# Kernel optimization log

Hardware: AMD Instinct MI355X
Metric: run time of the kernel (lower is better)

The kernel has to match this reference:

```python
import jax, jax.numpy as jnp
import numpy as np

N = 500_000
D = 256
G = 1024


def setup_inputs() -> dict:
    key = jax.random.key(0)
    k1, k2, k3, k4, k5, k6 = jax.random.split(key, 6)
    x = jax.random.normal(k1, (N, D), dtype=jnp.float32)
    batch = jnp.sort(jax.random.randint(k2, (N,), 0, G).astype(jnp.int64))
    s = 1.0 / np.sqrt(D)
    W1 = jax.random.normal(k3, (D, D), dtype=jnp.float32) * s
    b1 = jax.random.normal(k4, (D,), dtype=jnp.float32) * 0.01
    W2 = jax.random.normal(k5, (D, 1), dtype=jnp.float32) * s
    b2 = jax.random.normal(k6, (1,), dtype=jnp.float32) * 0.01
    return {"x": x, "batch": batch, "num_graphs": G,
            "W1": W1, "b1": b1, "W2": W2, "b2": b2}


def reference(x, batch, num_graphs, W1, b1, W2, b2):
    # gate MLP: Linear -> Tanh -> Linear  => [N, 1]
    h = jnp.tanh(x @ W1 + b1)
    scores = (h @ W2 + b2)[:, 0]  # [N]
    # segment softmax over nodes grouped by graph id
    seg_max = jax.ops.segment_max(scores, batch, num_segments=num_graphs)  # [G]
    # empty segments give -inf max, but no node indexes them
    e = jnp.exp(scores - seg_max[batch])  # [N]
    denom = jax.ops.segment_sum(e, batch, num_segments=num_graphs)  # [G]
    attn = e / denom[batch]  # [N]
    weighted = x * attn[:, None]  # [N, D]
    # global_add_pool: scatter-add nodes into graphs
    return jax.ops.segment_sum(weighted, batch, num_segments=num_graphs)  # [G, D]
```

## Files before the change

kernel.cpp:

```cpp
#include <hip/hip_runtime.h>
#include <hip/hip_bf16.h>

#define D 256

typedef __attribute__((ext_vector_type(8))) short bf16x8;
typedef __attribute__((ext_vector_type(4))) float f32x4;

__device__ __forceinline__ unsigned short f2bf(float a) {
    unsigned int u = __float_as_uint(a);
    u = (u + 0x7fffu + ((u >> 16) & 1u)) >> 16;
    return (unsigned short)u;
}

__device__ __forceinline__ unsigned int cvt_pk_bf16(float a, float b) {
    unsigned int r;
    asm("v_cvt_pk_bf16_f32 %0, %1, %2" : "=v"(r) : "v"(a), "v"(b));
    return r;
}

__device__ __forceinline__ float fast_tanh(float v) {
    float a = __builtin_fabsf(v);
    float e = __builtin_amdgcn_exp2f(a * -2.88539008177793f);
    float t = (1.0f - e) * __builtin_amdgcn_rcpf(1.0f + e);
    return __builtin_copysignf(t, v);
}

__device__ __forceinline__ int xf_off(int c, int r, int q) {
    return ((c << 10) + (r << 5) + (q << 4)) ^ ((c & 3) << 5) ^ ((r & 4) << 2);
}

__global__ void pack_w1_k(const float* __restrict__ W1, unsigned short* __restrict__ W1p) {
    int p = blockIdx.x * 256 + threadIdx.x;
    int e  = p & 7;
    int l  = (p >> 3) & 63;
    int cb = (p >> 9) & 15;
    int kk = p >> 13;
    int k   = 32 * kk + 8 * (l >> 4) + e;
    int col = 16 * cb + (l & 15);
    W1p[p] = f2bf(W1[k * D + col]);
}

__global__ void zero_k(float* __restrict__ p, int n) {
    int i = blockIdx.x * 256 + threadIdx.x;
    if (i < n) p[i] = 0.f;
}

__global__ void __launch_bounds__(256, 4)
fused_k(const float* __restrict__ x,
        const unsigned short* __restrict__ W1p,
        const float* __restrict__ b1,
        const float* __restrict__ W2,
        const float* __restrict__ b2,
        const int* __restrict__ batch, int N,
        float* __restrict__ accb, float* __restrict__ den) {
    __shared__ __align__(16) float Xf[8192];
    __shared__ float red[4][256];
    __shared__ float scpart[4][32];
    __shared__ float erow[32];
    __shared__ int   bids[32];

    const int tid = threadIdx.x;
    const int w   = tid >> 6;
    const int l   = tid & 63;
    const int l15 = l & 15;
    const int g4  = l >> 4;
    const int row0 = blockIdx.x * 32;

    char* xb = reinterpret_cast<char*>(Xf);

    const float4* x4 = reinterpret_cast<const float4*>(x);
    const bool full = (row0 + 32 <= N);
    #pragma unroll
    for (int it = 0; it < 8; ++it) {
        int idx = it * 256 + tid;
        int r    = idx >> 6;
        int col4 = idx & 63;
        float4 v = make_float4(0.f, 0.f, 0.f, 0.f);
        if (full || row0 + r < N) v = x4[(size_t)(row0 + r) * 64 + col4];
        *reinterpret_cast<float4*>(xb + xf_off(col4 >> 1, r, col4 & 1)) = v;
    }
    if (tid < 32) bids[tid] = batch[min(row0 + tid, N - 1)];
    __syncthreads();

    f32x4 acc[2][4];
    #pragma unroll
    for (int m = 0; m < 2; ++m)
        #pragma unroll
        for (int n = 0; n < 4; ++n)
            acc[m][n] = (f32x4){0.f, 0.f, 0.f, 0.f};

    #pragma unroll
    for (int kk = 0; kk < 8; ++kk) {
        bf16x8 bfr[4];
        #pragma unroll
        for (int n = 0; n < 4; ++n) {
            const bf16x8* bp = reinterpret_cast<const bf16x8*>(
                W1p + (size_t)(((kk * 16) + (w * 4 + n)) * 64 + l) * 8);
            bfr[n] = *bp;
        }
        bf16x8 afr[2];
        #pragma unroll
        for (int m = 0; m < 2; ++m) {
            int r = 16 * m + l15;
            int c = 4 * kk + g4;
            int o0 = xf_off(c, r, 0);
            float4 f0 = *reinterpret_cast<const float4*>(xb + o0);
            float4 f1 = *reinterpret_cast<const float4*>(xb + (o0 ^ 16));
            uint4 u;
            u.x = cvt_pk_bf16(f0.x, f0.y);
            u.y = cvt_pk_bf16(f0.z, f0.w);
            u.z = cvt_pk_bf16(f1.x, f1.y);
            u.w = cvt_pk_bf16(f1.z, f1.w);
            afr[m] = *reinterpret_cast<bf16x8*>(&u);
        }
        #pragma unroll
        for (int m = 0; m < 2; ++m)
            #pragma unroll
            for (int n = 0; n < 4; ++n)
                acc[m][n] = __builtin_amdgcn_mfma_f32_16x16x32_bf16(afr[m], bfr[n], acc[m][n], 0, 0, 0);
    }

    float part[2][4];
    #pragma unroll
    for (int m = 0; m < 2; ++m)
        #pragma unroll
        for (int r = 0; r < 4; ++r) part[m][r] = 0.f;

    #pragma unroll
    for (int n = 0; n < 4; ++n) {
        int col = 64 * w + 16 * n + l15;
        float b1v = b1[col];
        float w2v = W2[col];
        #pragma unroll
        for (int m = 0; m < 2; ++m)
            #pragma unroll
            for (int r = 0; r < 4; ++r) {
                float h = fast_tanh(acc[m][n][r] + b1v);
                part[m][r] += h * w2v;
            }
    }

    #pragma unroll
    for (int m = 0; m < 2; ++m)
        #pragma unroll
        for (int r = 0; r < 4; ++r) {
            float p = part[m][r];
            p += __shfl_xor(p, 8, 16);
            p += __shfl_xor(p, 4, 16);
            p += __shfl_xor(p, 2, 16);
            p += __shfl_xor(p, 1, 16);
            if (l15 == 0) scpart[w][16 * m + 4 * g4 + r] = p;
        }
    __syncthreads();

    if (tid < 32) {
        float s = scpart[0][tid] + scpart[1][tid] + scpart[2][tid] + scpart[3][tid] + b2[0];
        erow[tid] = (row0 + tid < N)
                  ? __builtin_amdgcn_exp2f(s * 1.4426950408889634f)
                  : 0.f;
    }
    __syncthreads();

    const int g0 = bids[0], g1 = bids[31];
    const int pc = l >> 1;
    const int pq = l & 1;
    for (int g = g0; g <= g1; ++g) {
        float4 a = make_float4(0.f, 0.f, 0.f, 0.f);
        #pragma unroll
        for (int it = 0; it < 8; ++it) {
            int r = 4 * it + w;
            float e = (bids[r] == g) ? erow[r] : 0.f;
            float4 v = *reinterpret_cast<const float4*>(xb + xf_off(pc, r, pq));
            a.x += e * v.x;
            a.y += e * v.y;
            a.z += e * v.z;
            a.w += e * v.w;
        }
        red[w][l * 4 + 0] = a.x;
        red[w][l * 4 + 1] = a.y;
        red[w][l * 4 + 2] = a.z;
        red[w][l * 4 + 3] = a.w;
        __syncthreads();
        float s = red[0][tid] + red[1][tid] + red[2][tid] + red[3][tid];
        atomicAdd(&accb[(size_t)g * D + tid], s);
        if (w == 0) {
            float e = 0.f;
            if (l < 32) e = (bids[l] == g) ? erow[l] : 0.f;
            e += __shfl_xor(e, 32);
            e += __shfl_xor(e, 16);
            e += __shfl_xor(e, 8);
            e += __shfl_xor(e, 4);
            e += __shfl_xor(e, 2);
            e += __shfl_xor(e, 1);
            if (l == 0) atomicAdd(&den[g], e);
        }
        __syncthreads();
    }
}

__global__ void __launch_bounds__(256)
norm_k(const float* __restrict__ accb, const float* __restrict__ den,
       float* __restrict__ out) {
    int g = blockIdx.x;
    float dv = den[g];
    float inv = (dv > 0.f) ? 1.0f / dv : 0.f;
    out[(size_t)g * D + threadIdx.x] = accb[(size_t)g * D + threadIdx.x] * inv;
}

extern "C" void kernel_launch(void* const* d_in, const int* in_sizes, int n_in,
                              void* d_out, int out_size, void* d_ws, size_t ws_size,
                              hipStream_t stream) {
    const float* x     = (const float*)d_in[0];
    const int*   batch = (const int*)d_in[1];
    const float* W1    = (const float*)d_in[3];
    const float* b1    = (const float*)d_in[4];
    const float* W2    = (const float*)d_in[5];
    const float* b2    = (const float*)d_in[6];
    float* out = (float*)d_out;

    const int N = in_sizes[0] / D;
    const int G = out_size / D;

    char* ws = (char*)d_ws;
    unsigned short* W1p = (unsigned short*)ws;
    float* accb = (float*)(ws + 131072);
    float* den  = (float*)(ws + 131072 + (size_t)G * D * 4);

    zero_k<<<dim3((G * D + G + 255) / 256), dim3(256), 0, stream>>>(accb, G * D + G);
    pack_w1_k<<<dim3(256), dim3(256), 0, stream>>>(W1, W1p);
    fused_k<<<dim3((N + 31) / 32), dim3(256), 0, stream>>>(x, W1p, b1, W2, b2, batch, N, accb, den);
    norm_k<<<dim3(G), dim3(256), 0, stream>>>(accb, den, out);
}
```

Measured before the change: 226.7 us.

## Persistent fused kernel with double-buffered async x loads and cross-tile segment accumulation

Replaces the one-block-per-32-rows launch with a persistent grid of 512 blocks, each walking a contiguous range of tiles. W1 fragments, b1 and W2 are loaded into registers once per block, and the next tile of x is prefetched into a second LDS buffer through direct global-to-LDS loads while the current tile runs its MFMA work. Pooling partials carry across tiles and are flushed with atomics only when the graph id changes, which cuts the number of atomics and barriers per tile. The cost is higher register pressure from 32 resident B fragments and 64KB of LDS, which lowers occupancy to 2 blocks per CU, plus more complex barrier logic.

```diff
diff --git a/kernel.cpp b/kernel.cpp
--- a/kernel.cpp
+++ b/kernel.cpp
@@ -1,7 +1,8 @@
 #include <hip/hip_runtime.h>
-#include <hip/hip_bf16.h>
 
 #define D 256
+#define ROWS 32
+#define NBLK 512
 
 typedef __attribute__((ext_vector_type(8))) short bf16x8;
 typedef __attribute__((ext_vector_type(4))) float f32x4;
@@ -27,6 +28,12 @@
 
 __device__ __forceinline__ int xf_off(int c, int r, int q) {
     return ((c << 10) + (r << 5) + (q << 4)) ^ ((c & 3) << 5) ^ ((r & 4) << 2);
+}
+
+__device__ __forceinline__ void gload_lds16(const void* g, void* l) {
+    __builtin_amdgcn_global_load_lds(
+        (const __attribute__((address_space(1))) unsigned int*)g,
+        (__attribute__((address_space(3))) unsigned int*)l, 16, 0, 0);
 }
 
 __global__ void pack_w1_k(const float* __restrict__ W1, unsigned short* __restrict__ W1p) {
@@ -45,157 +52,222 @@
     if (i < n) p[i] = 0.f;
 }
 
-__global__ void __launch_bounds__(256, 4)
+#define STAGE(XN, tn) do {                                                      \
+    const int _r0s = (tn) * ROWS;                                               \
+    _Pragma("unroll")                                                           \
+    for (int _it = 0; _it < 8; ++_it) {                                         \
+        const int _c = _it * 4 + w;                                             \
+        const int _r = (l >> 1) ^ (_c & 3);                                     \
+        const int _q = (l & 1) ^ ((_r >> 2) & 1);                               \
+        int _row = _r0s + _r; _row = (_row < N) ? _row : (N - 1);               \
+        gload_lds16((const char*)x + ((size_t)_row << 10) + (size_t)(((_c << 1) + _q) << 4), \
+                    (char*)(XN) + (_it << 12) + (w << 10) + (l << 4));          \
+    }                                                                           \
+} while (0)
+
+#define FLUSHX() do {                                                           \
+    *reinterpret_cast<float4*>(&red[w][l * 4]) = a4;                            \
+    int _m8 = 0x7fffffff;                                                       \
+    _Pragma("unroll")                                                           \
+    for (int _it = 0; _it < 8; ++_it)                                           \
+        if (bg[_it] > g_cur && bg[_it] < _m8) _m8 = bg[_it];                    \
+    _m8 = min(_m8, __shfl_xor(_m8, 1));  _m8 = min(_m8, __shfl_xor(_m8, 2));    \
+    _m8 = min(_m8, __shfl_xor(_m8, 4));  _m8 = min(_m8, __shfl_xor(_m8, 8));    \
+    _m8 = min(_m8, __shfl_xor(_m8, 16)); _m8 = min(_m8, __shfl_xor(_m8, 32));   \
+    float _dw = den_p;                                                          \
+    _dw += __shfl_xor(_dw, 1);  _dw += __shfl_xor(_dw, 2);                      \
+    _dw += __shfl_xor(_dw, 4);  _dw += __shfl_xor(_dw, 8);                      \
+    _dw += __shfl_xor(_dw, 16); _dw += __shfl_xor(_dw, 32);                     \
+    if (l == 0) { gmin4[w] = _m8; denw[w] = _dw; }                              \
+    asm volatile("s_waitcnt lgkmcnt(0)" ::: "memory");                          \
+    __builtin_amdgcn_sched_barrier(0);                                          \
+    __builtin_amdgcn_s_barrier();                                               \
+    __builtin_amdgcn_sched_barrier(0);                                          \
+    { const float _fs = red[0][tid] + red[1][tid] + red[2][tid] + red[3][tid];  \
+      atomicAdd(&accb[(size_t)g_cur * D + tid], _fs); }                         \
+    if (tid == 0)                                                               \
+        atomicAdd(&den[g_cur], (denw[0] + denw[1] + denw[2] + denw[3]) * 0.015625f); \
+    gnv = min(min(gmin4[0], gmin4[1]), min(gmin4[2], gmin4[3]));                \
+    a4 = make_float4(0.f, 0.f, 0.f, 0.f); den_p = 0.f;                          \
+    __builtin_amdgcn_s_barrier();                                               \
+    __builtin_amdgcn_sched_barrier(0);                                          \
+} while (0)
+
+#define POOL(XC) do {                                                           \
+    if (g_cur < 0) g_cur = g0u;                                                 \
+    while (true) {                                                              \
+        _Pragma("unroll")                                                       \
+        for (int _it = 0; _it < 8; ++_it) {                                     \
+            const int _r = 4 * _it + w;                                         \
+            const float _e = (bg[_it] == g_cur) ? erow[_r] : 0.f;               \
+            const float4 _v = *reinterpret_cast<const float4*>(                 \
+                (const char*)(XC) + xf_off(l >> 1, _r, l & 1));                 \
+            a4.x += _e * _v.x; a4.y += _e * _v.y;                               \
+            a4.z += _e * _v.z; a4.w += _e * _v.w;                               \
+            den_p += _e;                                                        \
+        }                                                                       \
+        if (glast <= g_cur) break;                                              \
+        FLUSHX();                                                               \
+        g_cur = gnv;                                                            \
+    }                                                                           \
+} while (0)
+
+#define BODY(XC, XN) do {                                                       \
+    const int _row0 = t * ROWS;                                                 \
+    _Pragma("unroll")                                                           \
+    for (int _it = 0; _it < 8; ++_it) {                                         \
+        int _ri = _row0 + 4 * _it + w;                                          \
+        bg[_it] = batch[_ri < N ? _ri : N - 1];                                 \
+    }                                                                           \
+    const int g0u = batch[_row0];                                               \
+    int _gli = _row0 + 31;                                                      \
+    const int glast = batch[_gli < N ? _gli : N - 1];                           \
+    __builtin_amdgcn_sched_barrier(0);                                          \
+    const bool _hn = (t + 1 < t1);                                              \
+    if (_hn) {                                                                  \
+        STAGE(XN, t + 1);                                                       \
+        asm volatile("s_waitcnt vmcnt(8) lgkmcnt(0)" ::: "memory");             \
+    } else {                                                                    \
+        asm volatile("s_waitcnt vmcnt(0) lgkmcnt(0)" ::: "memory");             \
+    }                                                                           \
+    __builtin_amdgcn_sched_barrier(0);                                          \
+    __builtin_amdgcn_s_barrier();                                               \
+    __builtin_amdgcn_sched_barrier(0);                                          \
+     \
+    f32x4 acc[2][4];                                                            \
+    _Pragma("unroll")                                                           \
+    for (int _m = 0; _m < 2; ++_m)                                              \
+        _Pragma("unroll")                                                       \
+        for (int _n = 0; _n < 4; ++_n) acc[_m][_n] = (f32x4){0.f, 0.f, 0.f, 0.f}; \
+    _Pragma("unroll")                                                           \
+    for (int _kk = 0; _kk < 8; ++_kk) {                                         \
+        bf16x8 _afr[2];                                                         \
+        _Pragma("unroll")                                                       \
+        for (int _m = 0; _m < 2; ++_m) {                                        \
+            const int _rr = 16 * _m + l15;                                      \
+            const int _cc = 4 * _kk + g4;                                       \
+            const int _o0 = xf_off(_cc, _rr, 0);                                \
+            const float4 _f0 = *reinterpret_cast<const float4*>((const char*)(XC) + _o0); \
+            const float4 _f1 = *reinterpret_cast<const float4*>((const char*)(XC) + (_o0 ^ 16)); \
+            uint4 _u;                                                           \
+            _u.x = cvt_pk_bf16(_f0.x, _f0.y); _u.y = cvt_pk_bf16(_f0.z, _f0.w); \
+            _u.z = cvt_pk_bf16(_f1.x, _f1.y); _u.w = cvt_pk_bf16(_f1.z, _f1.w); \
+            _afr[_m] = *reinterpret_cast<bf16x8*>(&_u);                         \
+        }                                                                       \
+        _Pragma("unroll")                                                       \
+        for (int _m = 0; _m < 2; ++_m)                                          \
+            _Pragma("unroll")                                                   \
+            for (int _n = 0; _n < 4; ++_n)                                      \
+                acc[_m][_n] = __builtin_amdgcn_mfma_f32_16x16x32_bf16(          \
+                    _afr[_m], bfr[_kk * 4 + _n], acc[_m][_n], 0, 0, 0);         \
+    }                                                                           \
+    {                                                                           \
+        float _part[2][4];                                                      \
+        _Pragma("unroll")                                                       \
+        for (int _m = 0; _m < 2; ++_m)                                          \
+            _Pragma("unroll")                                                   \
+            for (int _r = 0; _r < 4; ++_r) _part[_m][_r] = 0.f;                 \
+        _Pragma("unroll")                                                       \
+        for (int _n = 0; _n < 4; ++_n)                                          \
+            _Pragma("unroll")                                                   \
+            for (int _m = 0; _m < 2; ++_m)                                      \
+                _Pragma("unroll")                                               \
+                for (int _r = 0; _r < 4; ++_r) {                                \
+                    float _h = fast_tanh(acc[_m][_n][_r] + b1v[_n]);            \
+                    _part[_m][_r] += _h * w2v[_n];                              \
+                }                                                               \
+        _Pragma("unroll")                                                       \
+        for (int _m = 0; _m < 2; ++_m)                                          \
+            _Pragma("unroll")                                                   \
+            for (int _r = 0; _r < 4; ++_r) {                                    \
+                float _p = _part[_m][_r];                                       \
+                _p += __shfl_xor(_p, 8, 16); _p += __shfl_xor(_p, 4, 16);       \
+                _p += __shfl_xor(_p, 2, 16); _p += __shfl_xor(_p, 1, 16);       \
+                if (l15 == 0) scpart[w][16 * _m + 4 * g4 + _r] = _p;            \
+            }                                                                   \
+    }                                                                           \
+    asm volatile("s_waitcnt lgkmcnt(0)" ::: "memory");                          \
+    __builtin_amdgcn_sched_barrier(0);                                          \
+    __builtin_amdgcn_s_barrier();                                               \
+    __builtin_amdgcn_sched_barrier(0);                                          \
+    if (tid < 32) {                                                             \
+        float _s = scpart[0][tid] + scpart[1][tid] + scpart[2][tid] + scpart[3][tid] + b2v; \
+        erow[tid] = ((_row0 + tid) < N)                                         \
+                  ? __builtin_amdgcn_exp2f(_s * 1.4426950408889634f) : 0.f;     \
+    }                                                                           \
+    asm volatile("s_waitcnt lgkmcnt(0)" ::: "memory");                          \
+    __builtin_amdgcn_sched_barrier(0);                                          \
+    __builtin_amdgcn_s_barrier();                                               \
+    __builtin_amdgcn_sched_barrier(0);                                          \
+    POOL(XC);                                                                   \
+    asm volatile("s_waitcnt lgkmcnt(0)" ::: "memory");                          \
+    __builtin_amdgcn_sched_barrier(0);                                          \
+    __builtin_amdgcn_s_barrier();                                               \
+    __builtin_amdgcn_sched_barrier(0);                                          \
+    ++t;                                                                        \
+} while (0)
+
+__global__ void __launch_bounds__(256, 2)
 fused_k(const float* __restrict__ x,
         const unsigned short* __restrict__ W1p,
         const float* __restrict__ b1,
         const float* __restrict__ W2,
         const float* __restrict__ b2,
-        const int* __restrict__ batch, int N,
+        const int* __restrict__ batch,
+        int N, int NT,
         float* __restrict__ accb, float* __restrict__ den) {
-    __shared__ __align__(16) float Xf[8192];
-    __shared__ float red[4][256];
+    __shared__ __align__(16) char Xf0[32768];
+    __shared__ __align__(16) char Xf1[32768];
+    __shared__ __align__(16) float red[4][256];
     __shared__ float scpart[4][32];
     __shared__ float erow[32];
-    __shared__ int   bids[32];
+    __shared__ int   gmin4[4];
+    __shared__ float denw[4];
 
     const int tid = threadIdx.x;
     const int w   = tid >> 6;
     const int l   = tid & 63;
     const int l15 = l & 15;
     const int g4  = l >> 4;
-    const int row0 = blockIdx.x * 32;
-
-    char* xb = reinterpret_cast<char*>(Xf);
-
-    const float4* x4 = reinterpret_cast<const float4*>(x);
-    const bool full = (row0 + 32 <= N);
+
+    const int tpb = (NT + NBLK - 1) / NBLK;
+    int t = blockIdx.x * tpb;
+    const int t1 = min(NT, t + tpb);
+    if (t >= t1) return;
+
+    bf16x8 bfr[32];
     #pragma unroll
-    for (int it = 0; it < 8; ++it) {
-        int idx = it * 256 + tid;
-        int r    = idx >> 6;
-        int col4 = idx & 63;
-        float4 v = make_float4(0.f, 0.f, 0.f, 0.f);
-        if (full || row0 + r < N) v = x4[(size_t)(row0 + r) * 64 + col4];
-        *reinterpret_cast<float4*>(xb + xf_off(col4 >> 1, r, col4 & 1)) = v;
-    }
-    if (tid < 32) bids[tid] = batch[min(row0 + tid, N - 1)];
-    __syncthreads();
-
-    f32x4 acc[2][4];
-    #pragma unroll
-    for (int m = 0; m < 2; ++m)
+    for (int kk = 0; kk < 8; ++kk)
         #pragma unroll
         for (int n = 0; n < 4; ++n)
-            acc[m][n] = (f32x4){0.f, 0.f, 0.f, 0.f};
-
-    #pragma unroll
-    for (int kk = 0; kk < 8; ++kk) {
-        bf16x8 bfr[4];
-        #pragma unroll
-        for (int n = 0; n < 4; ++n) {
-            const bf16x8* bp = reinterpret_cast<const bf16x8*>(
+            bfr[kk * 4 + n] = *reinterpret_cast<const bf16x8*>(
                 W1p + (size_t)(((kk * 16) + (w * 4 + n)) * 64 + l) * 8);
-            bfr[n] = *bp;
-        }
-        bf16x8 afr[2];
-        #pragma unroll
-        for (int m = 0; m < 2; ++m) {
-            int r = 16 * m + l15;
-            int c = 4 * kk + g4;
-            int o0 = xf_off(c, r, 0);
-            float4 f0 = *reinterpret_cast<const float4*>(xb + o0);
-            float4 f1 = *reinterpret_cast<const float4*>(xb + (o0 ^ 16));
-            uint4 u;
-            u.x = cvt_pk_bf16(f0.x, f0.y);
-            u.y = cvt_pk_bf16(f0.z, f0.w);
-            u.z = cvt_pk_bf16(f1.x, f1.y);
-            u.w = cvt_pk_bf16(f1.z, f1.w);
-            afr[m] = *reinterpret_cast<bf16x8*>(&u);
-        }
-        #pragma unroll
-        for (int m = 0; m < 2; ++m)
-            #pragma unroll
-            for (int n = 0; n < 4; ++n)
-                acc[m][n] = __builtin_amdgcn_mfma_f32_16x16x32_bf16(afr[m], bfr[n], acc[m][n], 0, 0, 0);
-    }
-
-    float part[2][4];
-    #pragma unroll
-    for (int m = 0; m < 2; ++m)
-        #pragma unroll
-        for (int r = 0; r < 4; ++r) part[m][r] = 0.f;
-
+
+    float b1v[4], w2v[4];
     #pragma unroll
     for (int n = 0; n < 4; ++n) {
         int col = 64 * w + 16 * n + l15;
-        float b1v = b1[col];
-        float w2v = W2[col];
-        #pragma unroll
-        for (int m = 0; m < 2; ++m)
-            #pragma unroll
-            for (int r = 0; r < 4; ++r) {
-                float h = fast_tanh(acc[m][n][r] + b1v);
-                part[m][r] += h * w2v;
-            }
+        b1v[n] = b1[col];
+        w2v[n] = W2[col];
     }
-
-    #pragma unroll
-    for (int m = 0; m < 2; ++m)
-        #pragma unroll
-        for (int r = 0; r < 4; ++r) {
-            float p = part[m][r];
-            p += __shfl_xor(p, 8, 16);
-            p += __shfl_xor(p, 4, 16);
-            p += __shfl_xor(p, 2, 16);
-            p += __shfl_xor(p, 1, 16);
-            if (l15 == 0) scpart[w][16 * m + 4 * g4 + r] = p;
-        }
-    __syncthreads();
-
-    if (tid < 32) {
-        float s = scpart[0][tid] + scpart[1][tid] + scpart[2][tid] + scpart[3][tid] + b2[0];
-        erow[tid] = (row0 + tid < N)
-                  ? __builtin_amdgcn_exp2f(s * 1.4426950408889634f)
-                  : 0.f;
+    const float b2v = b2[0];
+
+    STAGE(Xf0, t);
+
+    float4 a4 = make_float4(0.f, 0.f, 0.f, 0.f);
+    float den_p = 0.f;
+    int g_cur = -1;
+    int gnv = 0;
+    int bg[8];
+
+    while (true) {
+        BODY(Xf0, Xf1);
+        if (t >= t1) break;
+        BODY(Xf1, Xf0);
+        if (t >= t1) break;
     }
-    __syncthreads();
-
-    const int g0 = bids[0], g1 = bids[31];
-    const int pc = l >> 1;
-    const int pq = l & 1;
-    for (int g = g0; g <= g1; ++g) {
-        float4 a = make_float4(0.f, 0.f, 0.f, 0.f);
-        #pragma unroll
-        for (int it = 0; it < 8; ++it) {
-            int r = 4 * it + w;
-            float e = (bids[r] == g) ? erow[r] : 0.f;
-            float4 v = *reinterpret_cast<const float4*>(xb + xf_off(pc, r, pq));
-            a.x += e * v.x;
-            a.y += e * v.y;
-            a.z += e * v.z;
-            a.w += e * v.w;
-        }
-        red[w][l * 4 + 0] = a.x;
-        red[w][l * 4 + 1] = a.y;
-        red[w][l * 4 + 2] = a.z;
-        red[w][l * 4 + 3] = a.w;
-        __syncthreads();
-        float s = red[0][tid] + red[1][tid] + red[2][tid] + red[3][tid];
-        atomicAdd(&accb[(size_t)g * D + tid], s);
-        if (w == 0) {
-            float e = 0.f;
-            if (l < 32) e = (bids[l] == g) ? erow[l] : 0.f;
-            e += __shfl_xor(e, 32);
-            e += __shfl_xor(e, 16);
-            e += __shfl_xor(e, 8);
-            e += __shfl_xor(e, 4);
-            e += __shfl_xor(e, 2);
-            e += __shfl_xor(e, 1);
-            if (l == 0) atomicAdd(&den[g], e);
-        }
-        __syncthreads();
-    }
+
+    FLUSHX();
 }
 
 __global__ void __launch_bounds__(256)
@@ -220,6 +292,7 @@
 
     const int N = in_sizes[0] / D;
     const int G = out_size / D;
+    const int NT = (N + ROWS - 1) / ROWS;
 
     char* ws = (char*)d_ws;
     unsigned short* W1p = (unsigned short*)ws;
@@ -228,6 +301,7 @@
 
     zero_k<<<dim3((G * D + G + 255) / 256), dim3(256), 0, stream>>>(accb, G * D + G);
     pack_w1_k<<<dim3(256), dim3(256), 0, stream>>>(W1, W1p);
-    fused_k<<<dim3((N + 31) / 32), dim3(256), 0, stream>>>(x, W1p, b1, W2, b2, batch, N, accb, den);
+    fused_k<<<dim3(min(NBLK, NT)), dim3(256), 0, stream>>>(x, W1p, b1, W2, b2, batch,
+                                                           N, NT, accb, den);
     norm_k<<<dim3(G), dim3(256), 0, stream>>>(accb, den, out);
 }
```

Measured after the change: 189.2 us. 16.5% less time.
